# Performance work log

Hardware: AMD Instinct MI355X
Metric: run time of the kernel (lower is better)

The kernel has to match this reference:

```python
import jax, jax.numpy as jnp
import numpy as np

N, E, D, SD, SH, EA, FC, H = 50000, 800000, 128, 64, 16, 32, 128, 8
EPS = 1e-5


def setup_inputs() -> dict:
    key = jax.random.key(0)
    ks = jax.random.split(key, 20)
    rn = lambda k, shp, fan: jax.random.normal(k, shp, jnp.float32) / np.sqrt(fan).astype(np.float32)
    return {
        'node_features': jax.random.normal(ks[0], (N, D), jnp.float32),
        'edge_attr': jax.random.normal(ks[1], (E, EA), jnp.float32),
        'edge_sh': jax.random.normal(ks[2], (E, SH), jnp.float32),
        'W_node': rn(ks[3], (D, D), D),
        'fc1': rn(ks[4], (EA, FC), EA), 'b1': jnp.zeros((FC,), jnp.float32),
        'fc2': rn(ks[5], (FC, FC), FC), 'b2': jnp.zeros((FC,), jnp.float32),
        'fc3': rn(ks[6], (FC, D), FC), 'b3': jnp.zeros((D,), jnp.float32),
        'W_sh': rn(ks[7], (SH, D), SH),
        'aW1': rn(ks[8], (2 * SD + EA, FC), 2 * SD + EA), 'ab1': jnp.zeros((FC,), jnp.float32),
        'aW2': rn(ks[9], (FC, FC), FC), 'ab2': jnp.zeros((FC,), jnp.float32),
        'aW3': rn(ks[10], (FC, H), FC), 'ab3': jnp.zeros((H,), jnp.float32),
        'W_out': rn(ks[11], (D, D), D),
        'edge_index': jax.random.randint(ks[12], (2, E), 0, N, jnp.int32),
        'batch': jnp.zeros((N,), jnp.int32),
    }


def reference(node_features, edge_attr, edge_sh, W_node, fc1, b1, fc2, b2, fc3, b3,
              W_sh, aW1, ab1, aW2, ab2, aW3, ab3, W_out, edge_index, batch):
    src, dst = edge_index[0], edge_index[1]
    x_src = node_features[src]                          # [E, D] gather
    # SeparableFCTP message MLP: radial FC net gates a depthwise TP with edge_sh
    h = jax.nn.silu(edge_attr @ fc1 + b1)
    h = jax.nn.silu(h @ fc2 + b2)
    scale = h @ fc3 + b3                                # [E, D] per-channel radial weights
    msg = jax.nn.silu((x_src @ W_node) * scale + edge_sh @ W_sh)  # [E, D]
    # edge attention over scalar channels (softmax over the edge dim, as in source)
    alpha_in = jnp.concatenate([x_src[:, :SD], node_features[dst, :SD], edge_attr], axis=-1)
    a = jax.nn.silu(alpha_in @ aW1 + ab1)
    a = jax.nn.silu(a @ aW2 + ab2)
    a = a @ aW3 + ab3                                   # [E, H]
    alpha = jax.nn.softmax(a, axis=0)
    alpha_mean = alpha.mean(axis=1, keepdims=True)      # [E, 1]
    agg = jax.ops.segment_sum(msg * alpha_mean, dst, num_segments=node_features.shape[0])
    out = node_features + agg @ W_out                   # dropout is identity in eval
    mu = out.mean(axis=-1, keepdims=True)
    var = out.var(axis=-1, keepdims=True)
    return (out - mu) / jnp.sqrt(var + EPS)
```

## Files before the change

kernel.cpp:

```cpp
#include <hip/hip_runtime.h>
#include <math.h>

#define N_NODES 50000
#define N_EDGES 800000
#define DIM     128
#define SDIM    64
#define SH_DIM  16
#define EA_DIM  32
#define FC_DIM  128
#define H_HEADS 8
#define AIN_DIM 160
#define LN_EPS  1e-5f

typedef __attribute__((ext_vector_type(8))) short short8;
typedef __attribute__((ext_vector_type(4))) short short4v;
typedef __attribute__((ext_vector_type(4))) float f32x4;

#define FR_FC1 0
#define FR_FC2 512
#define FR_FC3 2560
#define FR_WND 4608
#define FR_WSH 6656
#define FR_AW1 7168
#define FR_AW2 9728
#define FR_AW3 11776
#define FR_TOTAL 12032


__device__ __forceinline__ float silu(float x) {
    return x * __builtin_amdgcn_rcpf(1.0f + __expf(-x));
}

__device__ __forceinline__ unsigned short f2bf(float x) {
    unsigned u = __float_as_uint(x);
    return (unsigned short)((u + 0x7FFFu + ((u >> 16) & 1u)) >> 16);
}
__device__ __forceinline__ float bf2f(unsigned short h) { return __uint_as_float(((unsigned)h) << 16); }

__device__ __forceinline__ unsigned int fmap(float f) {
    unsigned int b = __float_as_uint(f);
    return (b & 0x80000000u) ? ~b : (b | 0x80000000u);
}
__device__ __forceinline__ float funmap(unsigned int u) {
    return (u & 0x80000000u) ? __uint_as_float(u & 0x7FFFFFFFu) : __uint_as_float(~u);
}

template<int KSTEPS, int STRIDE>
__device__ __forceinline__ void mm_col(const char* aBase, int lane, int ct0,
                                       const short8* __restrict__ bfrag, f32x4 (*acc)[2])
{
    const int l15  = lane & 15;
    const int koff = (lane >> 4) << 4;
    #pragma unroll
    for (int ks = 0; ks < KSTEPS; ++ks) {
        const short8 b0 = bfrag[(ks * 8 + ct0) * 64 + lane];
        const short8 b1 = bfrag[(ks * 8 + ct0 + 1) * 64 + lane];
        #pragma unroll
        for (int rs = 0; rs < 4; ++rs) {
            const int row = rs * 16 + l15;
            const short8 a = *(const short8*)(aBase + ((row * STRIDE + ks * 64 + koff) ^ ((row & 7) << 4)));
            acc[rs][0] = __builtin_amdgcn_mfma_f32_16x16x32_bf16(a, b0, acc[rs][0], 0, 0, 0);
            acc[rs][1] = __builtin_amdgcn_mfma_f32_16x16x32_bf16(a, b1, acc[rs][1], 0, 0, 0);
        }
    }
}

template<int KSTEPS, int NT, int STRIDE>
__device__ __forceinline__ void mm_acc(const char* aBase, int rowBase, int lane,
                                       const short8* __restrict__ bfrag, f32x4* acc)
{
    const int row  = rowBase + (lane & 15);
    const int swz  = (row & 7) << 4;
    const int rb   = row * STRIDE;
    const int koff = (lane >> 4) << 4;
    #pragma unroll
    for (int ks = 0; ks < KSTEPS; ++ks) {
        short8 a = *(const short8*)(aBase + ((rb + ks * 64 + koff) ^ swz));
        #pragma unroll
        for (int ct = 0; ct < NT; ++ct) {
            short8 b = bfrag[(ks * NT + ct) * 64 + lane];
            acc[ct] = __builtin_amdgcn_mfma_f32_16x16x32_bf16(a, b, acc[ct], 0, 0, 0);
        }
    }
}

template<int STRIDE>
__device__ __forceinline__ void store_col_silu(char* base, int lane, int ct0,
                                               f32x4 (*acc)[2], const float* __restrict__ bias)
{
    const int l15  = lane & 15;
    const float bv0 = bias[ct0 * 16 + l15];
    const float bv1 = bias[ct0 * 16 + 16 + l15];
    #pragma unroll
    for (int rs = 0; rs < 4; ++rs) {
        #pragma unroll
        for (int r = 0; r < 4; ++r) {
            const int row = rs * 16 + ((lane >> 4) << 2) + r;
            const int swz = (row & 7) << 4;
            const float v0 = silu(acc[rs][0][r] + bv0);
            const float v1 = silu(acc[rs][1][r] + bv1);
            *(short*)(base + ((row * STRIDE + ct0 * 32 + l15 * 2) ^ swz))      = (short)f2bf(v0);
            *(short*)(base + ((row * STRIDE + ct0 * 32 + 32 + l15 * 2) ^ swz)) = (short)f2bf(v1);
        }
    }
}

__device__ __forceinline__ void zerocol(f32x4 (*a)[2]) {
    #pragma unroll
    for (int i = 0; i < 4; ++i) {
        a[i][0] = (f32x4){0.f, 0.f, 0.f, 0.f};
        a[i][1] = (f32x4){0.f, 0.f, 0.f, 0.f};
    }
}

__global__ void k_prep(const float* __restrict__ fc1, const float* __restrict__ fc2,
                       const float* __restrict__ fc3, const float* __restrict__ W_node,
                       const float* __restrict__ W_sh, const float* __restrict__ aW1,
                       const float* __restrict__ aW2, const float* __restrict__ aW3,
                       short8* __restrict__ frags)
{
    const int gid = blockIdx.x * 256 + threadIdx.x;
    const float* src; int Ksrc, Nsrc, Nld, NT, base;
    if (gid < 2560) {
        if (gid < 512)  { src = fc1;  Ksrc = 32;  Nsrc = 128; Nld = 128; NT = 8; base = FR_FC1; }
        else            { src = fc2;  Ksrc = 128; Nsrc = 128; Nld = 128; NT = 8; base = FR_FC2; }
    } else if (gid < 6656) {
        if (gid < 4608) { src = fc3;    Ksrc = 128; Nsrc = 128; Nld = 128; NT = 8; base = FR_FC3; }
        else            { src = W_node; Ksrc = 128; Nsrc = 128; Nld = 128; NT = 8; base = FR_WND; }
    } else if (gid < 9728) {
        if (gid < 7168) { src = W_sh; Ksrc = 16;  Nsrc = 128; Nld = 128; NT = 8; base = FR_WSH; }
        else            { src = aW1;  Ksrc = 160; Nsrc = 128; Nld = 128; NT = 8; base = FR_AW1; }
    } else {
        if (gid < 11776){ src = aW2;  Ksrc = 128; Nsrc = 128; Nld = 128; NT = 8; base = FR_AW2; }
        else            { src = aW3;  Ksrc = 128; Nsrc = 8;   Nld = 8;   NT = 1; base = FR_AW3; }
    }
    const int local = gid - base;
    const int lane = local & 63;
    const int tmp  = local >> 6;
    const int ct   = tmp % NT;
    const int ks   = tmp / NT;
    const int col  = ct * 16 + (lane & 15);
    const int k0   = ks * 32 + ((lane >> 4) << 3);
    unsigned short o[8];
    #pragma unroll
    for (int i = 0; i < 8; ++i) {
        const int k = k0 + i;
        const float v = (k < Ksrc && col < Nsrc) ? src[(size_t)k * Nld + col] : 0.f;
        o[i] = f2bf(v);
    }
    unsigned a = (unsigned)o[0] | ((unsigned)o[1] << 16);
    unsigned b = (unsigned)o[2] | ((unsigned)o[3] << 16);
    unsigned c = (unsigned)o[4] | ((unsigned)o[5] << 16);
    unsigned d = (unsigned)o[6] | ((unsigned)o[7] << 16);
    ((uint4*)frags)[gid] = make_uint4(a, b, c, d);
}

__global__ void k_prep2(const float* __restrict__ nodef, unsigned short* __restrict__ nodefB)
{
    const int i = blockIdx.x * 256 + threadIdx.x;
    float4 v = ((const float4*)nodef)[i];
    short4v h = {(short)f2bf(v.x), (short)f2bf(v.y), (short)f2bf(v.z), (short)f2bf(v.w)};
    ((short4v*)nodefB)[i] = h;
}

__global__ void k0_init(float* __restrict__ aggz, unsigned int* __restrict__ cmax,
                        float* __restrict__ csum)
{
    const int total = N_NODES * (DIM / 2);
    for (int i = blockIdx.x * blockDim.x + threadIdx.x; i < total;
         i += gridDim.x * blockDim.x)
        aggz[i] = 0.0f;
    if (blockIdx.x == 0 && threadIdx.x < H_HEADS) {
        cmax[threadIdx.x] = fmap(-3.0e38f);
        csum[threadIdx.x] = 0.0f;
    }
}

__global__ __launch_bounds__(256, 2) void k1_logits(
    const unsigned short* __restrict__ nodefB, const float* __restrict__ eattr,
    const float* __restrict__ ab1, const float* __restrict__ ab2,
    const float* __restrict__ ab3,
    const short8* __restrict__ frags,
    const int* __restrict__ srcp, const int* __restrict__ dstp,
    unsigned short* __restrict__ a_outB, unsigned int* __restrict__ cmax)
{
    __shared__ __align__(16) char sBuf[64 * 512 + 64 * 256];
    char* sAIN = sBuf;
    char* sG1  = sBuf + 64 * 512;
    char* sG2  = sBuf;
    __shared__ int sid[64], did[64];
    __shared__ float wmaxL[32];

    const int tid = threadIdx.x;
    const int e0  = blockIdx.x * 64;

    if (tid < 64)            sid[tid]      = srcp[e0 + tid];
    else if (tid < 128)      did[tid - 64] = dstp[e0 + tid - 64];
    __syncthreads();

    for (int idx = tid; idx < 64 * 24; idx += 256) {
        const int e = idx / 24, q = idx - e * 24;
        if (q < 16) {
            const int node = (q < 8) ? sid[e] : did[e];
            const int qq = q & 7;
            short8 v = ((const short8*)(nodefB + (size_t)node * DIM))[qq];
            const int k = (q < 8 ? 0 : 64) + qq * 8;
            *(short8*)(sAIN + ((e * 512 + k * 2) ^ ((e & 7) << 4))) = v;
        } else {
            float4 v = ((const float4*)(eattr + (size_t)(e0 + e) * EA_DIM))[q - 16];
            short4v h = {(short)f2bf(v.x), (short)f2bf(v.y), (short)f2bf(v.z), (short)f2bf(v.w)};
            const int k = 128 + (q - 16) * 4;
            *(short4v*)(sAIN + ((e * 512 + k * 2) ^ ((e & 7) << 4))) = h;
        }
    }
    __syncthreads();

    const int lane = tid & 63, w = tid >> 6;
    const int ct0 = w * 2;
    f32x4 acc[4][2];

    zerocol(acc);
    mm_col<5, 512>(sAIN, lane, ct0, frags + FR_AW1, acc);
    store_col_silu<256>(sG1, lane, ct0, acc, ab1);
    __syncthreads();

    zerocol(acc);
    mm_col<4, 256>(sG1, lane, ct0, frags + FR_AW2, acc);
    store_col_silu<256>(sG2, lane, ct0, acc, ab2);
    __syncthreads();

    f32x4 p = {0.f, 0.f, 0.f, 0.f};
    mm_acc<4, 1, 256>(sG2, w * 16, lane, frags + FR_AW3, &p);

    const int h = lane & 15;
    float vmax = -3.0e38f;
    if (h < H_HEADS) {
        const float ab = ab3[h];
        #pragma unroll
        for (int r = 0; r < 4; ++r) {
            const int row = w * 16 + ((lane >> 4) << 2) + r;
            const unsigned short bv = f2bf(p[r] + ab);
            a_outB[(size_t)(e0 + row) * H_HEADS + h] = bv;
            vmax = fmaxf(vmax, bf2f(bv));
        }
    }
    vmax = fmaxf(vmax, __shfl_xor(vmax, 16));
    vmax = fmaxf(vmax, __shfl_xor(vmax, 32));
    if (lane < 8) wmaxL[w * 8 + lane] = vmax;
    __syncthreads();
    if (tid < 8) {
        const float m = fmaxf(fmaxf(wmaxL[tid], wmaxL[8 + tid]),
                              fmaxf(wmaxL[16 + tid], wmaxL[24 + tid]));
        atomicMax(&cmax[tid], fmap(m));
    }
}

__global__ void k2_expsum(const unsigned* __restrict__ a_bufB,
                          const unsigned int* __restrict__ cmax,
                          float* __restrict__ csum)
{
    __shared__ float partial[4][8];
    const int tid = threadIdx.x;
    const int p   = tid & 3;
    const float M0 = funmap(cmax[2 * p]);
    const float M1 = funmap(cmax[2 * p + 1]);
    float s0 = 0.f, s1 = 0.f;
    const int total = N_EDGES * 4;
    const int stride = gridDim.x * 256;
    for (int i = blockIdx.x * 256 + tid; i < total; i += stride) {
        const unsigned v = a_bufB[i];
        s0 += __expf(bf2f((unsigned short)(v & 0xFFFFu)) - M0);
        s1 += __expf(bf2f((unsigned short)(v >> 16)) - M1);
    }
    s0 += __shfl_xor(s0, 4);  s1 += __shfl_xor(s1, 4);
    s0 += __shfl_xor(s0, 8);  s1 += __shfl_xor(s1, 8);
    s0 += __shfl_xor(s0, 16); s1 += __shfl_xor(s1, 16);
    s0 += __shfl_xor(s0, 32); s1 += __shfl_xor(s1, 32);
    const int wave = tid >> 6, lane = tid & 63;
    if (lane < 4) { partial[wave][lane * 2] = s0; partial[wave][lane * 2 + 1] = s1; }
    __syncthreads();
    if (tid < 8) {
        float t = partial[0][tid] + partial[1][tid] + partial[2][tid] + partial[3][tid];
        atomicAdd(&csum[tid], t);
    }
}

__global__ __launch_bounds__(256, 2) void k3_message(
    const unsigned short* __restrict__ nodefB, const float* __restrict__ eattr,
    const float* __restrict__ esh,
    const float* __restrict__ b1, const float* __restrict__ b2,
    const float* __restrict__ b3,
    const short8* __restrict__ frags,
    const int* __restrict__ srcp, const int* __restrict__ dstp,
    const unsigned short* __restrict__ a_bufB, const unsigned int* __restrict__ cmax,
    const float* __restrict__ csum,
    unsigned short* __restrict__ aggB)
{
    __shared__ __align__(16) char sBuf[49152];
    char* sXS = sBuf;
    char* sEA = sBuf + 16384;
    char* sSH = sBuf + 24576;
    char* sH1 = sBuf + 32768;
    char* sH2 = sBuf + 16384;
    __shared__ float amL[64];
    __shared__ int sidL[64], didL[64];

    const int tid = threadIdx.x;
    const int e0  = blockIdx.x * 64;

    if (tid < 64)       sidL[tid]      = srcp[e0 + tid];
    else if (tid < 128) didL[tid - 64] = dstp[e0 + tid - 64];
    __syncthreads();

    for (int idx = tid; idx < 64 * 16; idx += 256) {
        const int e = idx >> 4, q = idx & 15;
        short8 v = ((const short8*)(nodefB + (size_t)sidL[e] * DIM))[q];
        *(short8*)(sXS + ((e * 256 + q * 16) ^ ((e & 7) << 4))) = v;
    }
    for (int idx = tid; idx < 64 * 8; idx += 256) {
        const int e = idx >> 3, q = idx & 7;
        float4 v = ((const float4*)(eattr + (size_t)(e0 + e) * EA_DIM))[q];
        short4v h = {(short)f2bf(v.x), (short)f2bf(v.y), (short)f2bf(v.z), (short)f2bf(v.w)};
        *(short4v*)(sEA + ((e * 128 + q * 8) ^ ((e & 7) << 4))) = h;
    }
    for (int idx = tid; idx < 64 * 8; idx += 256) {
        const int e = idx >> 3, q = idx & 7;
        short4v h = {0, 0, 0, 0};
        if (q < 4) {
            float4 v = ((const float4*)(esh + (size_t)(e0 + e) * SH_DIM))[q];
            h = (short4v){(short)f2bf(v.x), (short)f2bf(v.y), (short)f2bf(v.z), (short)f2bf(v.w)};
        }
        *(short4v*)(sSH + ((e * 128 + q * 8) ^ ((e & 7) << 4))) = h;
    }
    if (tid < 64) {
        uint4 v = ((const uint4*)a_bufB)[e0 + tid];
        const unsigned short* pv = (const unsigned short*)&v;
        float s = 0.f;
        #pragma unroll
        for (int h = 0; h < H_HEADS; ++h)
            s += __expf(bf2f(pv[h]) - funmap(cmax[h])) * __builtin_amdgcn_rcpf(csum[h]);
        amL[tid] = s * (1.0f / H_HEADS);
    }
    __syncthreads();

    const int lane = tid & 63, w = tid >> 6;
    const int ct0 = w * 2, l15 = lane & 15;
    f32x4 sw[4][2], sc[4][2], xw[4][2];

    zerocol(sw);
    mm_col<1, 128>(sSH, lane, ct0, frags + FR_WSH, sw);
    zerocol(sc);
    mm_col<1, 128>(sEA, lane, ct0, frags + FR_FC1, sc);
    store_col_silu<256>(sH1, lane, ct0, sc, b1);
    __syncthreads();

    zerocol(sc);
    mm_col<4, 256>(sH1, lane, ct0, frags + FR_FC2, sc);
    store_col_silu<256>(sH2, lane, ct0, sc, b2);
    __syncthreads();

    zerocol(sc);
    mm_col<4, 256>(sH2, lane, ct0, frags + FR_FC3, sc);
    zerocol(xw);
    mm_col<4, 256>(sXS, lane, ct0, frags + FR_WND, xw);

    const float bv0 = b3[ct0 * 16 + l15];
    const float bv1 = b3[ct0 * 16 + 16 + l15];

    #pragma unroll
    for (int rs = 0; rs < 4; ++rs) {
        #pragma unroll
        for (int r = 0; r < 4; ++r) {
            const int row = rs * 16 + ((lane >> 4) << 2) + r;
            const float am = amL[row];
            const float m0 = silu(xw[rs][0][r] * (sc[rs][0][r] + bv0) + sw[rs][0][r]) * am;
            const float m1 = silu(xw[rs][1][r] * (sc[rs][1][r] + bv1) + sw[rs][1][r]) * am;
            const unsigned u  = (unsigned)f2bf(m0) | ((unsigned)f2bf(m1) << 16);
            const unsigned un = __shfl_xor(u, 1);
            if (!(lane & 1)) {
                const unsigned p0 = (u & 0xFFFFu) | (un << 16);
                const unsigned p1 = (u >> 16) | (un & 0xFFFF0000u);
                const unsigned long long abase =
                    (unsigned long long)aggB + (unsigned long long)didL[row] * (DIM * 2);
                const unsigned long long a0 = abase + (unsigned)((ct0 * 16 + l15) * 2);
                const unsigned long long a1 = abase + (unsigned)((ct0 * 16 + 16 + l15) * 2);
                asm volatile("global_atomic_pk_add_bf16 %0, %1, off" :: "v"(a0), "v"(p0) : "memory");
                asm volatile("global_atomic_pk_add_bf16 %0, %1, off" :: "v"(a1), "v"(p1) : "memory");
            }
        }
    }
}

#define K4_NB 16

__global__ __launch_bounds__(256, 2) void k4_out(
    const float* __restrict__ nodef, const unsigned short* __restrict__ aggB,
    const float* __restrict__ W_out, float* __restrict__ outp)
{
    __shared__ float aggL[K4_NB * 132];
    __shared__ float outL[K4_NB * 144];
    const int tid = threadIdx.x;
    const int n0  = blockIdx.x * K4_NB;

    for (int idx = tid; idx < K4_NB * 16; idx += 256) {
        const int nl = idx >> 4, q = idx & 15;
        uint4 v = ((const uint4*)(aggB))[(size_t)(n0 + nl) * 16 + q];
        float* dstp = aggL + nl * 132 + q * 8;
        dstp[0] = bf2f((unsigned short)(v.x & 0xFFFF)); dstp[1] = bf2f((unsigned short)(v.x >> 16));
        dstp[2] = bf2f((unsigned short)(v.y & 0xFFFF)); dstp[3] = bf2f((unsigned short)(v.y >> 16));
        dstp[4] = bf2f((unsigned short)(v.z & 0xFFFF)); dstp[5] = bf2f((unsigned short)(v.z >> 16));
        dstp[6] = bf2f((unsigned short)(v.w & 0xFFFF)); dstp[7] = bf2f((unsigned short)(v.w >> 16));
    }
    __syncthreads();

    const int f = tid & 127, ng = tid >> 7;
    float acc[8];
    #pragma unroll
    for (int j = 0; j < 8; ++j) acc[j] = nodef[(size_t)(n0 + ng * 8 + j) * DIM + f];
    #pragma unroll 4
    for (int k = 0; k < DIM; ++k) {
        const float wv = W_out[(size_t)k * DIM + f];
        #pragma unroll
        for (int j = 0; j < 8; ++j) acc[j] += aggL[(ng * 8 + j) * 132 + k] * wv;
    }
    #pragma unroll
    for (int j = 0; j < 8; ++j) outL[(ng * 8 + j) * 144 + f] = acc[j];
    __syncthreads();

    const int node = tid >> 4, l16 = tid & 15;
    float v[8];
    float s = 0.f;
    #pragma unroll
    for (int j = 0; j < 8; ++j) { v[j] = outL[node * 144 + l16 + j * 16]; s += v[j]; }
    #pragma unroll
    for (int m = 1; m < 16; m <<= 1) s += __shfl_xor(s, m);
    const float mu = s * (1.0f / DIM);
    float vs = 0.f;
    #pragma unroll
    for (int j = 0; j < 8; ++j) { const float d = v[j] - mu; vs += d * d; }
    #pragma unroll
    for (int m = 1; m < 16; m <<= 1) vs += __shfl_xor(vs, m);
    const float rstd = rsqrtf(vs * (1.0f / DIM) + LN_EPS);
    #pragma unroll
    for (int j = 0; j < 8; ++j)
        outp[(size_t)(n0 + node) * DIM + l16 + j * 16] = (v[j] - mu) * rstd;
}

extern "C" void kernel_launch(void* const* d_in, const int* in_sizes, int n_in,
                              void* d_out, int out_size, void* d_ws, size_t ws_size,
                              hipStream_t stream)
{
    const float* nodef  = (const float*)d_in[0];
    const float* eattr  = (const float*)d_in[1];
    const float* esh    = (const float*)d_in[2];
    const float* W_node = (const float*)d_in[3];
    const float* fc1    = (const float*)d_in[4];
    const float* b1     = (const float*)d_in[5];
    const float* fc2    = (const float*)d_in[6];
    const float* b2     = (const float*)d_in[7];
    const float* fc3    = (const float*)d_in[8];
    const float* b3     = (const float*)d_in[9];
    const float* W_sh   = (const float*)d_in[10];
    const float* aW1    = (const float*)d_in[11];
    const float* ab1    = (const float*)d_in[12];
    const float* aW2    = (const float*)d_in[13];
    const float* ab2    = (const float*)d_in[14];
    const float* aW3    = (const float*)d_in[15];
    const float* ab3    = (const float*)d_in[16];
    const float* W_out  = (const float*)d_in[17];
    const int*   eidx   = (const int*)d_in[18];
    const int* srcp = eidx;
    const int* dstp = eidx + N_EDGES;

    float* ws = (float*)d_ws;
    unsigned short* aggB  = (unsigned short*)ws;
    unsigned int*   cmax  = (unsigned int*)(ws + 3200000);
    float*          csum  = ws + 3200008;
    unsigned short* a_bufB = (unsigned short*)(ws + 3200016);
    short8*         frags = (short8*)(ws + 6400016);
    unsigned short* nodefB = (unsigned short*)(ws + 6448144);
    float* outp = (float*)d_out;

    k_prep    <<<47, 256, 0, stream>>>(fc1, fc2, fc3, W_node, W_sh, aW1, aW2, aW3, frags);
    k_prep2   <<<N_NODES * DIM / 4 / 256, 256, 0, stream>>>(nodef, nodefB);
    k0_init   <<<2048, 256, 0, stream>>>((float*)aggB, cmax, csum);
    k1_logits <<<N_EDGES / 64, 256, 0, stream>>>(nodefB, eattr, ab1, ab2, ab3, frags,
                                                 srcp, dstp, a_bufB, cmax);
    k2_expsum <<<1024, 256, 0, stream>>>((const unsigned*)a_bufB, cmax, csum);
    k3_message<<<N_EDGES / 64, 256, 0, stream>>>(nodefB, eattr, esh, b1, b2, b3, frags,
                                                 srcp, dstp, a_bufB, cmax, csum, aggB);
    k4_out    <<<N_NODES / K4_NB, 256, 0, stream>>>(nodef, aggB, W_out, outp);
}
```

Before: 868.5 us.

## Precompute per-node projections to replace per-edge node matmuls with gathers

Result: faster. 822.1 us (-5.3%).

```diff
diff --git a/kernel.cpp b/kernel.cpp
--- a/kernel.cpp
+++ b/kernel.cpp
@@ -9,28 +9,27 @@
 #define EA_DIM  32
 #define FC_DIM  128
 #define H_HEADS 8
-#define AIN_DIM 160
 #define LN_EPS  1e-5f
 
 typedef __attribute__((ext_vector_type(8))) short short8;
-typedef __attribute__((ext_vector_type(4))) short short4v;
 typedef __attribute__((ext_vector_type(4))) float f32x4;
 
-#define FR_FC1 0
-#define FR_FC2 512
-#define FR_FC3 2560
-#define FR_WND 4608
-#define FR_WSH 6656
-#define FR_AW1 7168
-#define FR_AW2 9728
-#define FR_AW3 11776
+#define FR_FC1   0
+#define FR_FC2   512
+#define FR_FC3   2560
+#define FR_WND   4608
+#define FR_WSH   6656
+#define FR_AW1EA 7168
+#define FR_AW1A  7680
+#define FR_AW1B  8704
+#define FR_AW2   9728
+#define FR_AW3   11776
 #define FR_TOTAL 12032
 
 
 __device__ __forceinline__ float silu(float x) {
     return x * __builtin_amdgcn_rcpf(1.0f + __expf(-x));
 }
-
 __device__ __forceinline__ unsigned short f2bf(float x) {
     unsigned u = __float_as_uint(x);
     return (unsigned short)((u + 0x7FFFu + ((u >> 16) & 1u)) >> 16);
@@ -44,8 +43,19 @@
 __device__ __forceinline__ float funmap(unsigned int u) {
     return (u & 0x80000000u) ? __uint_as_float(u & 0x7FFFFFFFu) : __uint_as_float(~u);
 }
-
-template<int KSTEPS, int STRIDE>
+__device__ __forceinline__ uint4 pack8(float4 a, float4 b) {
+    return make_uint4((unsigned)f2bf(a.x) | ((unsigned)f2bf(a.y) << 16),
+                      (unsigned)f2bf(a.z) | ((unsigned)f2bf(a.w) << 16),
+                      (unsigned)f2bf(b.x) | ((unsigned)f2bf(b.y) << 16),
+                      (unsigned)f2bf(b.z) | ((unsigned)f2bf(b.w) << 16));
+}
+__device__ __forceinline__ unsigned addpk(unsigned a, unsigned b) {
+    float lo = bf2f((unsigned short)(a & 0xFFFFu)) + bf2f((unsigned short)(b & 0xFFFFu));
+    float hi = bf2f((unsigned short)(a >> 16))     + bf2f((unsigned short)(b >> 16));
+    return (unsigned)f2bf(lo) | ((unsigned)f2bf(hi) << 16);
+}
+
+template<int KSTEPS, int STRIDE, int SWZM>
 __device__ __forceinline__ void mm_col(const char* aBase, int lane, int ct0,
                                        const short8* __restrict__ bfrag, f32x4 (*acc)[2])
 {
@@ -58,7 +68,8 @@
         #pragma unroll
         for (int rs = 0; rs < 4; ++rs) {
             const int row = rs * 16 + l15;
-            const short8 a = *(const short8*)(aBase + ((row * STRIDE + ks * 64 + koff) ^ ((row & 7) << 4)));
+            const short8 a = *(const short8*)(aBase +
+                ((row * STRIDE + ks * 64 + koff) ^ ((row & SWZM) << 4)));
             acc[rs][0] = __builtin_amdgcn_mfma_f32_16x16x32_bf16(a, b0, acc[rs][0], 0, 0, 0);
             acc[rs][1] = __builtin_amdgcn_mfma_f32_16x16x32_bf16(a, b1, acc[rs][1], 0, 0, 0);
         }
@@ -84,7 +95,6 @@
     }
 }
 
-template<int STRIDE>
 __device__ __forceinline__ void store_col_silu(char* base, int lane, int ct0,
                                                f32x4 (*acc)[2], const float* __restrict__ bias)
 {
@@ -99,8 +109,23 @@
             const int swz = (row & 7) << 4;
             const float v0 = silu(acc[rs][0][r] + bv0);
             const float v1 = silu(acc[rs][1][r] + bv1);
-            *(short*)(base + ((row * STRIDE + ct0 * 32 + l15 * 2) ^ swz))      = (short)f2bf(v0);
-            *(short*)(base + ((row * STRIDE + ct0 * 32 + 32 + l15 * 2) ^ swz)) = (short)f2bf(v1);
+            *(short*)(base + ((row * 256 + ct0 * 32 + l15 * 2) ^ swz))      = (short)f2bf(v0);
+            *(short*)(base + ((row * 256 + ct0 * 32 + 32 + l15 * 2) ^ swz)) = (short)f2bf(v1);
+        }
+    }
+}
+
+__device__ __forceinline__ void store_col_raw(char* base, int lane, int ct0, f32x4 (*acc)[2])
+{
+    const int l15 = lane & 15;
+    #pragma unroll
+    for (int rs = 0; rs < 4; ++rs) {
+        #pragma unroll
+        for (int r = 0; r < 4; ++r) {
+            const int row = rs * 16 + ((lane >> 4) << 2) + r;
+            const int swz = (row & 7) << 4;
+            *(short*)(base + ((row * 256 + ct0 * 32 + l15 * 2) ^ swz))      = (short)f2bf(acc[rs][0][r]);
+            *(short*)(base + ((row * 256 + ct0 * 32 + 32 + l15 * 2) ^ swz)) = (short)f2bf(acc[rs][1][r]);
         }
     }
 }
@@ -117,22 +142,24 @@
                        const float* __restrict__ fc3, const float* __restrict__ W_node,
                        const float* __restrict__ W_sh, const float* __restrict__ aW1,
                        const float* __restrict__ aW2, const float* __restrict__ aW3,
-                       short8* __restrict__ frags)
+                       uint4* __restrict__ frags)
 {
     const int gid = blockIdx.x * 256 + threadIdx.x;
-    const float* src; int Ksrc, Nsrc, Nld, NT, base;
-    if (gid < 2560) {
-        if (gid < 512)  { src = fc1;  Ksrc = 32;  Nsrc = 128; Nld = 128; NT = 8; base = FR_FC1; }
-        else            { src = fc2;  Ksrc = 128; Nsrc = 128; Nld = 128; NT = 8; base = FR_FC2; }
-    } else if (gid < 6656) {
-        if (gid < 4608) { src = fc3;    Ksrc = 128; Nsrc = 128; Nld = 128; NT = 8; base = FR_FC3; }
-        else            { src = W_node; Ksrc = 128; Nsrc = 128; Nld = 128; NT = 8; base = FR_WND; }
+    const float* src; int Ksrc = 128, Nsrc = 128, Nld = 128, NT = 8, base, rowOff = 0;
+    if (gid < 4608) {
+        if (gid < 512)        { src = fc1;  Ksrc = 32;  base = FR_FC1; }
+        else if (gid < 2560)  { src = fc2;              base = FR_FC2; }
+        else                  { src = fc3;              base = FR_FC3; }
+    } else if (gid < 7168) {
+        if (gid < 6656)       { src = W_node;           base = FR_WND; }
+        else                  { src = W_sh; Ksrc = 16;  base = FR_WSH; }
     } else if (gid < 9728) {
-        if (gid < 7168) { src = W_sh; Ksrc = 16;  Nsrc = 128; Nld = 128; NT = 8; base = FR_WSH; }
-        else            { src = aW1;  Ksrc = 160; Nsrc = 128; Nld = 128; NT = 8; base = FR_AW1; }
+        if (gid < 7680)       { src = aW1; Ksrc = 32; rowOff = 128; base = FR_AW1EA; }
+        else if (gid < 8704)  { src = aW1; Ksrc = 64; rowOff = 0;   base = FR_AW1A; }
+        else                  { src = aW1; Ksrc = 64; rowOff = 64;  base = FR_AW1B; }
     } else {
-        if (gid < 11776){ src = aW2;  Ksrc = 128; Nsrc = 128; Nld = 128; NT = 8; base = FR_AW2; }
-        else            { src = aW3;  Ksrc = 128; Nsrc = 8;   Nld = 8;   NT = 1; base = FR_AW3; }
+        if (gid < 11776)      { src = aW2;              base = FR_AW2; }
+        else                  { src = aW3; Nsrc = 8; Nld = 8; NT = 1; base = FR_AW3; }
     }
     const int local = gid - base;
     const int lane = local & 63;
@@ -145,22 +172,68 @@
     #pragma unroll
     for (int i = 0; i < 8; ++i) {
         const int k = k0 + i;
-        const float v = (k < Ksrc && col < Nsrc) ? src[(size_t)k * Nld + col] : 0.f;
+        const float v = (k < Ksrc && col < Nsrc) ? src[(size_t)(rowOff + k) * Nld + col] : 0.f;
         o[i] = f2bf(v);
     }
-    unsigned a = (unsigned)o[0] | ((unsigned)o[1] << 16);
-    unsigned b = (unsigned)o[2] | ((unsigned)o[3] << 16);
-    unsigned c = (unsigned)o[4] | ((unsigned)o[5] << 16);
-    unsigned d = (unsigned)o[6] | ((unsigned)o[7] << 16);
-    ((uint4*)frags)[gid] = make_uint4(a, b, c, d);
-}
-
-__global__ void k_prep2(const float* __restrict__ nodef, unsigned short* __restrict__ nodefB)
-{
-    const int i = blockIdx.x * 256 + threadIdx.x;
-    float4 v = ((const float4*)nodef)[i];
-    short4v h = {(short)f2bf(v.x), (short)f2bf(v.y), (short)f2bf(v.z), (short)f2bf(v.w)};
-    ((short4v*)nodefB)[i] = h;
+    frags[gid] = make_uint4((unsigned)o[0] | ((unsigned)o[1] << 16),
+                            (unsigned)o[2] | ((unsigned)o[3] << 16),
+                            (unsigned)o[4] | ((unsigned)o[5] << 16),
+                            (unsigned)o[6] | ((unsigned)o[7] << 16));
+}
+
+__global__ __launch_bounds__(256, 2) void kP_node(
+    const float* __restrict__ nodef, const short8* __restrict__ frags,
+    uint4* __restrict__ XWB, uint4* __restrict__ P1B, uint4* __restrict__ P2B)
+{
+    __shared__ __align__(16) char sA[16384];
+    __shared__ __align__(16) char sO[16384];
+    const int tid = threadIdx.x;
+    const int n0  = blockIdx.x * 64;
+
+    #pragma unroll
+    for (int i = 0; i < 4; ++i) {
+        const int c = tid + 256 * i, r = c >> 4, q = c & 15;
+        int idx = n0 + r; if (idx >= N_NODES) idx = N_NODES - 1;
+        float4 a = ((const float4*)(nodef + (size_t)idx * DIM))[q * 2];
+        float4 b = ((const float4*)(nodef + (size_t)idx * DIM))[q * 2 + 1];
+        *(uint4*)(sA + ((r * 256 + q * 16) ^ ((r & 7) << 4))) = pack8(a, b);
+    }
+    __syncthreads();
+
+    const int lane = tid & 63, wv = tid >> 6, ct0 = wv * 2;
+    f32x4 acc[4][2];
+
+    zerocol(acc); mm_col<4, 256, 7>(sA, lane, ct0, frags + FR_WND, acc);
+    store_col_raw(sO, lane, ct0, acc);
+    __syncthreads();
+    #pragma unroll
+    for (int i = 0; i < 4; ++i) {
+        const int c = tid + 256 * i, r = c >> 4, q = c & 15;
+        if (n0 + r < N_NODES)
+            XWB[(size_t)(n0 + r) * 16 + q] = *(uint4*)(sO + ((r * 256 + q * 16) ^ ((r & 7) << 4)));
+    }
+    __syncthreads();
+
+    zerocol(acc); mm_col<2, 256, 7>(sA, lane, ct0, frags + FR_AW1A, acc);
+    store_col_raw(sO, lane, ct0, acc);
+    __syncthreads();
+    #pragma unroll
+    for (int i = 0; i < 4; ++i) {
+        const int c = tid + 256 * i, r = c >> 4, q = c & 15;
+        if (n0 + r < N_NODES)
+            P1B[(size_t)(n0 + r) * 16 + q] = *(uint4*)(sO + ((r * 256 + q * 16) ^ ((r & 7) << 4)));
+    }
+    __syncthreads();
+
+    zerocol(acc); mm_col<2, 256, 7>(sA, lane, ct0, frags + FR_AW1B, acc);
+    store_col_raw(sO, lane, ct0, acc);
+    __syncthreads();
+    #pragma unroll
+    for (int i = 0; i < 4; ++i) {
+        const int c = tid + 256 * i, r = c >> 4, q = c & 15;
+        if (n0 + r < N_NODES)
+            P2B[(size_t)(n0 + r) * 16 + q] = *(uint4*)(sO + ((r * 256 + q * 16) ^ ((r & 7) << 4)));
+    }
 }
 
 __global__ void k0_init(float* __restrict__ aggz, unsigned int* __restrict__ cmax,
@@ -176,69 +249,92 @@
     }
 }
 
-__global__ __launch_bounds__(256, 2) void k1_logits(
-    const unsigned short* __restrict__ nodefB, const float* __restrict__ eattr,
+__global__ __launch_bounds__(256, 4) void k1_logits(
+    const float* __restrict__ eattr,
     const float* __restrict__ ab1, const float* __restrict__ ab2,
     const float* __restrict__ ab3,
     const short8* __restrict__ frags,
     const int* __restrict__ srcp, const int* __restrict__ dstp,
+    const uint4* __restrict__ P1B, const uint4* __restrict__ P2B,
     unsigned short* __restrict__ a_outB, unsigned int* __restrict__ cmax)
 {
-    __shared__ __align__(16) char sBuf[64 * 512 + 64 * 256];
-    char* sAIN = sBuf;
-    char* sG1  = sBuf + 64 * 512;
-    char* sG2  = sBuf;
-    __shared__ int sid[64], did[64];
-    __shared__ float wmaxL[32];
+    __shared__ __align__(16) char sBuf[32768];
+    char* sG1 = sBuf;
+    char* sEA = sBuf + 12288;
+    char* R2  = sBuf + 16384;
+    float* wmaxL = (float*)R2;
 
     const int tid = threadIdx.x;
     const int e0  = blockIdx.x * 64;
 
-    if (tid < 64)            sid[tid]      = srcp[e0 + tid];
-    else if (tid < 128)      did[tid - 64] = dstp[e0 + tid - 64];
-    __syncthreads();
-
-    for (int idx = tid; idx < 64 * 24; idx += 256) {
-        const int e = idx / 24, q = idx - e * 24;
-        if (q < 16) {
-            const int node = (q < 8) ? sid[e] : did[e];
-            const int qq = q & 7;
-            short8 v = ((const short8*)(nodefB + (size_t)node * DIM))[qq];
-            const int k = (q < 8 ? 0 : 64) + qq * 8;
-            *(short8*)(sAIN + ((e * 512 + k * 2) ^ ((e & 7) << 4))) = v;
-        } else {
-            float4 v = ((const float4*)(eattr + (size_t)(e0 + e) * EA_DIM))[q - 16];
-            short4v h = {(short)f2bf(v.x), (short)f2bf(v.y), (short)f2bf(v.z), (short)f2bf(v.w)};
-            const int k = 128 + (q - 16) * 4;
-            *(short4v*)(sAIN + ((e * 512 + k * 2) ^ ((e & 7) << 4))) = h;
-        }
-    }
-    __syncthreads();
-
-    const int lane = tid & 63, w = tid >> 6;
-    const int ct0 = w * 2;
+    uint4 pa[4], pb[4];
+    #pragma unroll
+    for (int i = 0; i < 4; ++i) {
+        const int c = tid + 256 * i, e = c >> 4, q = c & 15;
+        const int s = srcp[e0 + e], d = dstp[e0 + e];
+        pa[i] = P1B[(size_t)s * 16 + q];
+        pb[i] = P2B[(size_t)d * 16 + q];
+    }
+    {
+        const int e = tid >> 2, q = tid & 3;
+        float4 a = ((const float4*)(eattr + (size_t)(e0 + e) * EA_DIM))[q * 2];
+        float4 b = ((const float4*)(eattr + (size_t)(e0 + e) * EA_DIM))[q * 2 + 1];
+        *(uint4*)(sEA + e * 64 + ((q * 16) ^ ((e & 3) << 4))) = pack8(a, b);
+    }
+    __syncthreads();
+
+    const int lane = tid & 63, wv = tid >> 6, ct0 = wv * 2, l15 = lane & 15;
     f32x4 acc[4][2];
 
     zerocol(acc);
-    mm_col<5, 512>(sAIN, lane, ct0, frags + FR_AW1, acc);
-    store_col_silu<256>(sG1, lane, ct0, acc, ab1);
+    mm_col<1, 64, 3>(sEA, lane, ct0, frags + FR_AW1EA, acc);
+    #pragma unroll
+    for (int i = 0; i < 4; ++i) {
+        const int c = tid + 256 * i, e = c >> 4, q = c & 15;
+        uint4 s;
+        s.x = addpk(pa[i].x, pb[i].x); s.y = addpk(pa[i].y, pb[i].y);
+        s.z = addpk(pa[i].z, pb[i].z); s.w = addpk(pa[i].w, pb[i].w);
+        *(uint4*)(R2 + ((e * 256 + q * 16) ^ ((e & 7) << 4))) = s;
+    }
+    __syncthreads();
+
+    {
+        const float bv0 = ab1[ct0 * 16 + l15];
+        const float bv1 = ab1[ct0 * 16 + 16 + l15];
+        const int c0 = ct0 * 32 + l15 * 2, c1 = c0 + 32;
+        #pragma unroll
+        for (int rs = 0; rs < 4; ++rs) {
+            #pragma unroll
+            for (int r = 0; r < 4; ++r) {
+                const int row = rs * 16 + ((lane >> 4) << 2) + r;
+                const int swz = (row & 7) << 4;
+                const float p0 = bf2f(*(const unsigned short*)(R2 + ((row * 256 + c0) ^ swz)));
+                const float p1 = bf2f(*(const unsigned short*)(R2 + ((row * 256 + c1) ^ swz)));
+                const float v0 = silu(acc[rs][0][r] + bv0 + p0);
+                const float v1 = silu(acc[rs][1][r] + bv1 + p1);
+                *(short*)(sG1 + ((row * 256 + c0) ^ swz)) = (short)f2bf(v0);
+                *(short*)(sG1 + ((row * 256 + c1) ^ swz)) = (short)f2bf(v1);
+            }
+        }
+    }
     __syncthreads();
 
     zerocol(acc);
-    mm_col<4, 256>(sG1, lane, ct0, frags + FR_AW2, acc);
-    store_col_silu<256>(sG2, lane, ct0, acc, ab2);
+    mm_col<4, 256, 7>(sG1, lane, ct0, frags + FR_AW2, acc);
+    store_col_silu(R2, lane, ct0, acc, ab2);
     __syncthreads();
 
     f32x4 p = {0.f, 0.f, 0.f, 0.f};
-    mm_acc<4, 1, 256>(sG2, w * 16, lane, frags + FR_AW3, &p);
-
-    const int h = lane & 15;
+    mm_acc<4, 1, 256>(R2, wv * 16, lane, frags + FR_AW3, &p);
+    __syncthreads();
+
+    const int h = l15;
     float vmax = -3.0e38f;
     if (h < H_HEADS) {
         const float ab = ab3[h];
         #pragma unroll
         for (int r = 0; r < 4; ++r) {
-            const int row = w * 16 + ((lane >> 4) << 2) + r;
+            const int row = wv * 16 + ((lane >> 4) << 2) + r;
             const unsigned short bv = f2bf(p[r] + ab);
             a_outB[(size_t)(e0 + row) * H_HEADS + h] = bv;
             vmax = fmaxf(vmax, bf2f(bv));
@@ -246,7 +342,7 @@
     }
     vmax = fmaxf(vmax, __shfl_xor(vmax, 16));
     vmax = fmaxf(vmax, __shfl_xor(vmax, 32));
-    if (lane < 8) wmaxL[w * 8 + lane] = vmax;
+    if (lane < 8) wmaxL[wv * 8 + lane] = vmax;
     __syncthreads();
     if (tid < 8) {
         const float m = fmaxf(fmaxf(wmaxL[tid], wmaxL[8 + tid]),
@@ -285,103 +381,104 @@
     }
 }
 
-__global__ __launch_bounds__(256, 2) void k3_message(
-    const unsigned short* __restrict__ nodefB, const float* __restrict__ eattr,
-    const float* __restrict__ esh,
+__global__ __launch_bounds__(256, 4) void k3_message(
+    const float* __restrict__ eattr, const float* __restrict__ esh,
     const float* __restrict__ b1, const float* __restrict__ b2,
     const float* __restrict__ b3,
     const short8* __restrict__ frags,
     const int* __restrict__ srcp, const int* __restrict__ dstp,
     const unsigned short* __restrict__ a_bufB, const unsigned int* __restrict__ cmax,
     const float* __restrict__ csum,
+    const uint4* __restrict__ XWB,
     unsigned short* __restrict__ aggB)
 {
-    __shared__ __align__(16) char sBuf[49152];
-    char* sXS = sBuf;
-    char* sEA = sBuf + 16384;
-    char* sSH = sBuf + 24576;
-    char* sH1 = sBuf + 32768;
-    char* sH2 = sBuf + 16384;
-    __shared__ float amL[64];
-    __shared__ int sidL[64], didL[64];
+    __shared__ __align__(16) char sBuf[32768];
+    char* R1 = sBuf;
+    char* R2 = sBuf + 16384;
+    __shared__ unsigned sMeta[64];
+    char* sEA = R2;
+    char* sSH = R2 + 4096;
 
     const int tid = threadIdx.x;
     const int e0  = blockIdx.x * 64;
 
-    if (tid < 64)       sidL[tid]      = srcp[e0 + tid];
-    else if (tid < 128) didL[tid - 64] = dstp[e0 + tid - 64];
-    __syncthreads();
-
-    for (int idx = tid; idx < 64 * 16; idx += 256) {
-        const int e = idx >> 4, q = idx & 15;
-        short8 v = ((const short8*)(nodefB + (size_t)sidL[e] * DIM))[q];
-        *(short8*)(sXS + ((e * 256 + q * 16) ^ ((e & 7) << 4))) = v;
-    }
-    for (int idx = tid; idx < 64 * 8; idx += 256) {
-        const int e = idx >> 3, q = idx & 7;
-        float4 v = ((const float4*)(eattr + (size_t)(e0 + e) * EA_DIM))[q];
-        short4v h = {(short)f2bf(v.x), (short)f2bf(v.y), (short)f2bf(v.z), (short)f2bf(v.w)};
-        *(short4v*)(sEA + ((e * 128 + q * 8) ^ ((e & 7) << 4))) = h;
-    }
-    for (int idx = tid; idx < 64 * 8; idx += 256) {
-        const int e = idx >> 3, q = idx & 7;
-        short4v h = {0, 0, 0, 0};
-        if (q < 4) {
-            float4 v = ((const float4*)(esh + (size_t)(e0 + e) * SH_DIM))[q];
-            h = (short4v){(short)f2bf(v.x), (short)f2bf(v.y), (short)f2bf(v.z), (short)f2bf(v.w)};
-        }
-        *(short4v*)(sSH + ((e * 128 + q * 8) ^ ((e & 7) << 4))) = h;
+    {
+        const int e = tid >> 2, q = tid & 3;
+        float4 a = ((const float4*)(eattr + (size_t)(e0 + e) * EA_DIM))[q * 2];
+        float4 b = ((const float4*)(eattr + (size_t)(e0 + e) * EA_DIM))[q * 2 + 1];
+        *(uint4*)(sEA + e * 64 + ((q * 16) ^ ((e & 3) << 4))) = pack8(a, b);
+        uint4 hz = make_uint4(0, 0, 0, 0);
+        if (q < 2) {
+            float4 c = ((const float4*)(esh + (size_t)(e0 + e) * SH_DIM))[q * 2];
+            float4 d = ((const float4*)(esh + (size_t)(e0 + e) * SH_DIM))[q * 2 + 1];
+            hz = pack8(c, d);
+        }
+        *(uint4*)(sSH + e * 64 + ((q * 16) ^ ((e & 3) << 4))) = hz;
     }
     if (tid < 64) {
-        uint4 v = ((const uint4*)a_bufB)[e0 + tid];
-        const unsigned short* pv = (const unsigned short*)&v;
+        uint4 av = ((const uint4*)a_bufB)[e0 + tid];
+        const unsigned short* pv = (const unsigned short*)&av;
         float s = 0.f;
         #pragma unroll
         for (int h = 0; h < H_HEADS; ++h)
             s += __expf(bf2f(pv[h]) - funmap(cmax[h])) * __builtin_amdgcn_rcpf(csum[h]);
-        amL[tid] = s * (1.0f / H_HEADS);
-    }
-    __syncthreads();
-
-    const int lane = tid & 63, w = tid >> 6;
-    const int ct0 = w * 2, l15 = lane & 15;
-    f32x4 sw[4][2], sc[4][2], xw[4][2];
+        sMeta[tid] = ((unsigned)dstp[e0 + tid] << 16) | (unsigned)f2bf(s * (1.0f / H_HEADS));
+    }
+    __syncthreads();
+
+    const int lane = tid & 63, wv = tid >> 6, ct0 = wv * 2, l15 = lane & 15;
+    f32x4 sw[4][2], acc[4][2];
 
     zerocol(sw);
-    mm_col<1, 128>(sSH, lane, ct0, frags + FR_WSH, sw);
-    zerocol(sc);
-    mm_col<1, 128>(sEA, lane, ct0, frags + FR_FC1, sc);
-    store_col_silu<256>(sH1, lane, ct0, sc, b1);
-    __syncthreads();
-
-    zerocol(sc);
-    mm_col<4, 256>(sH1, lane, ct0, frags + FR_FC2, sc);
-    store_col_silu<256>(sH2, lane, ct0, sc, b2);
-    __syncthreads();
-
-    zerocol(sc);
-    mm_col<4, 256>(sH2, lane, ct0, frags + FR_FC3, sc);
-    zerocol(xw);
-    mm_col<4, 256>(sXS, lane, ct0, frags + FR_WND, xw);
+    mm_col<1, 64, 3>(sSH, lane, ct0, frags + FR_WSH, sw);
+    zerocol(acc);
+    mm_col<1, 64, 3>(sEA, lane, ct0, frags + FR_FC1, acc);
+    store_col_silu(R1, lane, ct0, acc, b1);
+    __syncthreads();
+
+    uint4 xwc[4];
+    #pragma unroll
+    for (int i = 0; i < 4; ++i) {
+        const int c = tid + 256 * i, e = c >> 4, q = c & 15;
+        const int s = srcp[e0 + e];
+        xwc[i] = XWB[(size_t)s * 16 + q];
+    }
+    zerocol(acc);
+    mm_col<4, 256, 7>(R1, lane, ct0, frags + FR_FC2, acc);
+    store_col_silu(R2, lane, ct0, acc, b2);
+    __syncthreads();
+
+    #pragma unroll
+    for (int i = 0; i < 4; ++i) {
+        const int c = tid + 256 * i, e = c >> 4, q = c & 15;
+        *(uint4*)(R1 + ((e * 256 + q * 16) ^ ((e & 7) << 4))) = xwc[i];
+    }
+    zerocol(acc);
+    mm_col<4, 256, 7>(R2, lane, ct0, frags + FR_FC3, acc);
+    __syncthreads();
 
     const float bv0 = b3[ct0 * 16 + l15];
     const float bv1 = b3[ct0 * 16 + 16 + l15];
-
+    const int c0 = ct0 * 32 + l15 * 2, c1 = c0 + 32;
     #pragma unroll
     for (int rs = 0; rs < 4; ++rs) {
         #pragma unroll
         for (int r = 0; r < 4; ++r) {
             const int row = rs * 16 + ((lane >> 4) << 2) + r;
-            const float am = amL[row];
-            const float m0 = silu(xw[rs][0][r] * (sc[rs][0][r] + bv0) + sw[rs][0][r]) * am;
-            const float m1 = silu(xw[rs][1][r] * (sc[rs][1][r] + bv1) + sw[rs][1][r]) * am;
+            const int swz = (row & 7) << 4;
+            const unsigned meta = sMeta[row];
+            const float am = bf2f((unsigned short)(meta & 0xFFFFu));
+            const float xw0 = bf2f(*(const unsigned short*)(R1 + ((row * 256 + c0) ^ swz)));
+            const float xw1 = bf2f(*(const unsigned short*)(R1 + ((row * 256 + c1) ^ swz)));
+            const float m0 = silu(xw0 * (acc[rs][0][r] + bv0) + sw[rs][0][r]) * am;
+            const float m1 = silu(xw1 * (acc[rs][1][r] + bv1) + sw[rs][1][r]) * am;
             const unsigned u  = (unsigned)f2bf(m0) | ((unsigned)f2bf(m1) << 16);
             const unsigned un = __shfl_xor(u, 1);
             if (!(lane & 1)) {
                 const unsigned p0 = (u & 0xFFFFu) | (un << 16);
                 const unsigned p1 = (u >> 16) | (un & 0xFFFF0000u);
                 const unsigned long long abase =
-                    (unsigned long long)aggB + (unsigned long long)didL[row] * (DIM * 2);
+                    (unsigned long long)aggB + (unsigned long long)(meta >> 16) * (DIM * 2);
                 const unsigned long long a0 = abase + (unsigned)((ct0 * 16 + l15) * 2);
                 const unsigned long long a1 = abase + (unsigned)((ct0 * 16 + 16 + l15) * 2);
                 asm volatile("global_atomic_pk_add_bf16 %0, %1, off" :: "v"(a0), "v"(p0) : "memory");
@@ -473,21 +570,24 @@
     const int* dstp = eidx + N_EDGES;
 
     float* ws = (float*)d_ws;
-    unsigned short* aggB  = (unsigned short*)ws;
-    unsigned int*   cmax  = (unsigned int*)(ws + 3200000);
-    float*          csum  = ws + 3200008;
+    unsigned short* aggB   = (unsigned short*)ws;
+    unsigned int*   cmax   = (unsigned int*)(ws + 3200000);
+    float*          csum   = ws + 3200008;
     unsigned short* a_bufB = (unsigned short*)(ws + 3200016);
-    short8*         frags = (short8*)(ws + 6400016);
-    unsigned short* nodefB = (unsigned short*)(ws + 6448144);
+    uint4*          frags  = (uint4*)(ws + 6400016);
+    uint4*          XWB    = (uint4*)(ws + 6448144);
+    uint4*          P1B    = (uint4*)(ws + 9648144);
+    uint4*          P2B    = (uint4*)(ws + 12848144);
     float* outp = (float*)d_out;
 
     k_prep    <<<47, 256, 0, stream>>>(fc1, fc2, fc3, W_node, W_sh, aW1, aW2, aW3, frags);
-    k_prep2   <<<N_NODES * DIM / 4 / 256, 256, 0, stream>>>(nodef, nodefB);
+    kP_node   <<<(N_NODES + 63) / 64, 256, 0, stream>>>(nodef, (const short8*)frags,
+                                                        XWB, P1B, P2B);
     k0_init   <<<2048, 256, 0, stream>>>((float*)aggB, cmax, csum);
-    k1_logits <<<N_EDGES / 64, 256, 0, stream>>>(nodefB, eattr, ab1, ab2, ab3, frags,
-                                                 srcp, dstp, a_bufB, cmax);
+    k1_logits <<<N_EDGES / 64, 256, 0, stream>>>(eattr, ab1, ab2, ab3, (const short8*)frags,
+                                                 srcp, dstp, P1B, P2B, a_bufB, cmax);
     k2_expsum <<<1024, 256, 0, stream>>>((const unsigned*)a_bufB, cmax, csum);
-    k3_message<<<N_EDGES / 64, 256, 0, stream>>>(nodefB, eattr, esh, b1, b2, b3, frags,
-                                                 srcp, dstp, a_bufB, cmax, csum, aggB);
+    k3_message<<<N_EDGES / 64, 256, 0, stream>>>(eattr, esh, b1, b2, b3, (const short8*)frags,
+                                                 srcp, dstp, a_bufB, cmax, csum, XWB, aggB);
     k4_out    <<<N_NODES / K4_NB, 256, 0, stream>>>(nodef, aggB, W_out, outp);
 }
```
